# Kernel tuning notes

Measured on AMD Instinct MI355X. Metric: run time of the kernel, lower is better.

Reference implementation:

```python
import jax, jax.numpy as jnp
import numpy as np

H = 4          # num_heads (= num_kv_heads, num_kv_groups = 1)
DK = 256       # head_k_dim
DV = 256       # head_v_dim
M = 256        # num_slots
GATE_NORM = 16.0
EPS = 1e-5


def _rmsnorm(x, w):
    var = jnp.mean(jnp.square(x), axis=-1, keepdims=True)
    return x * jax.lax.rsqrt(var + EPS) * w


def _swish(x):
    return x * jax.nn.sigmoid(x)


def setup_inputs() -> dict:
    key = jax.random.key(0)
    ks = jax.random.split(key, 8)
    B, T, D = 4, 2048, 1024
    scale = 2 ** (-2.5) * (2.0 / (D + D)) ** 0.5 * (3.0 ** 0.5) * 2  # ~xavier*gain magnitude
    return {
        "hidden_states": jax.random.normal(ks[0], (B, T, D), jnp.float32),
        "norm_weight": jnp.ones((D,), jnp.float32),
        "w_q": jax.random.normal(ks[1], (D, D), jnp.float32) * scale,
        "w_k": jax.random.normal(ks[2], (D, D), jnp.float32) * scale,
        "w_v": jax.random.normal(ks[3], (D, D), jnp.float32) * scale,
        "w_f": jax.random.normal(ks[4], (H * M, D), jnp.float32) * scale,
        "gnorm_weight": jnp.ones((D,), jnp.float32),
        "w_o": jax.random.normal(ks[5], (D, D), jnp.float32) * scale,
    }


def _gsa_scan(q, k, v, s, g):
    # all inputs time-major: q [T,B,H,DK], k [T,B,H,DK], v [T,B,H,DV],
    # s [T,B,H,M] (slot write strength), g [T,B,H,M] (log forget gate)
    B, Hh = q.shape[1], q.shape[2]
    Hk0 = jnp.zeros((B, Hh, DK, M), q.dtype)
    Hv0 = jnp.zeros((B, Hh, M, DV), q.dtype)

    def step(carry, xs):
        Hk, Hv = carry
        qt, kt, vt, st, gt = xs
        lam = jnp.exp(gt)                                       # [B,H,M]
        # pass 1: linear attn over slots (gate on value/slot dim)
        Hk = Hk * lam[:, :, None, :] + kt[..., :, None] * st[..., None, :]
        z = jnp.einsum('bhk,bhkm->bhm', qt, Hk)                 # slot logits
        p = jax.nn.softmax(z, axis=-1)                          # slot read weights
        # pass 2: linear attn from slots to values (gate on key/slot dim)
        Hv = Hv * lam[..., :, None] + st[..., :, None] * vt[..., None, :]
        ot = jnp.einsum('bhm,bhmv->bhv', p, Hv)
        return (Hk, Hv), ot

    _, o = jax.lax.scan(step, (Hk0, Hv0), (q, k, v, s, g))
    return o  # [T,B,H,DV]


def reference(hidden_states, norm_weight, w_q, w_k, w_v, w_f, gnorm_weight, w_o):
    B, T, D = hidden_states.shape
    h = _rmsnorm(hidden_states, norm_weight)                    # norm_first
    q = _swish(h @ w_q.T).reshape(B, T, H, DK)                  # swish feature map
    k = _swish(h @ w_k.T).reshape(B, T, H, DK)
    v = _swish(h @ w_v.T).reshape(B, T, H, DV)
    f = jax.nn.log_sigmoid(h @ w_f.T).reshape(B, T, H, M) / GATE_NORM
    s = 1.0 - jnp.exp(f)
    tm = lambda x: jnp.transpose(x, (1, 0, 2, 3))               # [B,T,H,*] -> [T,B,H,*]
    o = _gsa_scan(tm(q), tm(k), tm(v), tm(s), tm(f))            # [T,B,H,DV]
    o = jnp.transpose(o, (1, 0, 2, 3)).reshape(B, T, H * DV)
    # use_norm & no output gate: swish -> RMSNorm -> o_proj
    o = _swish(o)
    o = _rmsnorm(o, gnorm_weight)
    return o @ w_o.T
```

## Files before the change

### kernel.cpp

```cpp
#include <hip/hip_runtime.h>
#include <hip/hip_bf16.h>

typedef unsigned short u16;
typedef unsigned int u32;

using bf16x8 = __bf16 __attribute__((ext_vector_type(8)));
using s16x8  = short  __attribute__((ext_vector_type(8)));
using f32x4  = float  __attribute__((ext_vector_type(4)));

#define DEV static __device__ __forceinline__

constexpr int T_ = 2048, D_ = 1024;
constexpr int C_ = 64, NC_ = 32;
constexpr float EPS_ = 1e-5f;

DEV float bf2f(u16 u) { return __uint_as_float(((u32)u) << 16); }
DEV u16 f2bf(float f) {
  u32 u = __float_as_uint(f);
  return (u16)((u + 0x7fffu + ((u >> 16) & 1u)) >> 16);
}
DEV float swishf(float x) { return x / (1.f + __expf(-x)); }
DEV f32x4 zero4() { f32x4 z = {0.f, 0.f, 0.f, 0.f}; return z; }

DEV bf16x8 ld8(const u16* p, int ld, int r0, int k0, int lane) {
  return *(const bf16x8*)(p + (size_t)(r0 + (lane & 15)) * ld +
                          (size_t)(k0 + ((lane >> 4) << 3)));
}
DEV f32x4 MFMA(bf16x8 a, bf16x8 b, f32x4 c) {
  return __builtin_amdgcn_mfma_f32_16x16x32_bf16(a, b, c, 0, 0, 0);
}
DEV void gld_lds16(const void* g, void* l) {
  __builtin_amdgcn_global_load_lds(
      (const __attribute__((address_space(1))) unsigned int*)g,
      (__attribute__((address_space(3))) unsigned int*)l, 16, 0, 0);
}

__global__ __launch_bounds__(256) void k_cvt5(
    const float* __restrict__ s0, const float* __restrict__ s1,
    const float* __restrict__ s2, const float* __restrict__ s3,
    const float* __restrict__ s4, u16* __restrict__ d0, u16* __restrict__ d1,
    u16* __restrict__ d2, u16* __restrict__ d3, u16* __restrict__ d4) {
  const int wsel = blockIdx.x >> 10;
  const float* s = (wsel == 0) ? s0 : (wsel == 1) ? s1 : (wsel == 2) ? s2
                   : (wsel == 3) ? s3 : s4;
  u16* d = (wsel == 0) ? d0 : (wsel == 1) ? d1 : (wsel == 2) ? d2
           : (wsel == 3) ? d3 : d4;
  const int i = (blockIdx.x & 1023) * 256 + threadIdx.x;
  float4 v = ((const float4*)s)[i];
  uint2 o;
  o.x = (u32)f2bf(v.x) | ((u32)f2bf(v.y) << 16);
  o.y = (u32)f2bf(v.z) | ((u32)f2bf(v.w) << 16);
  ((uint2*)d)[i] = o;
}

__global__ __launch_bounds__(256) void k_rmsnorm(const float* __restrict__ x,
                                                 const float* __restrict__ w,
                                                 u16* __restrict__ h) {
  const int row = blockIdx.x, tid = threadIdx.x;
  float4 v = ((const float4*)(x + (size_t)row * D_))[tid];
  float ss = v.x * v.x + v.y * v.y + v.z * v.z + v.w * v.w;
#pragma unroll
  for (int d = 32; d >= 1; d >>= 1) ss += __shfl_xor(ss, d, 64);
  __shared__ float red[4];
  if ((tid & 63) == 0) red[tid >> 6] = ss;
  __syncthreads();
  float rs = rsqrtf((red[0] + red[1] + red[2] + red[3]) * (1.f / D_) + EPS_);
  float4 wv = ((const float4*)w)[tid];
  uint2 o;
  o.x = (u32)f2bf(v.x * rs * wv.x) | ((u32)f2bf(v.y * rs * wv.y) << 16);
  o.y = (u32)f2bf(v.z * rs * wv.z) | ((u32)f2bf(v.w * rs * wv.w) << 16);
  *(uint2*)(h + (size_t)row * D_ + tid * 4) = o;
}

__global__ __launch_bounds__(256) void k_swishnorm(const u16* __restrict__ x,
                                                   const float* __restrict__ w,
                                                   u16* __restrict__ o) {
  const int row = blockIdx.x, tid = threadIdx.x;
  uint2 pk = *(const uint2*)(x + (size_t)row * D_ + tid * 4);
  float v0 = swishf(bf2f((u16)(pk.x & 0xffff))), v1 = swishf(bf2f((u16)(pk.x >> 16)));
  float v2 = swishf(bf2f((u16)(pk.y & 0xffff))), v3 = swishf(bf2f((u16)(pk.y >> 16)));
  float ss = v0 * v0 + v1 * v1 + v2 * v2 + v3 * v3;
#pragma unroll
  for (int d = 32; d >= 1; d >>= 1) ss += __shfl_xor(ss, d, 64);
  __shared__ float red[4];
  if ((tid & 63) == 0) red[tid >> 6] = ss;
  __syncthreads();
  float rs = rsqrtf((red[0] + red[1] + red[2] + red[3]) * (1.f / D_) + EPS_);
  float4 wv = ((const float4*)w)[tid];
  uint2 ov;
  ov.x = (u32)f2bf(v0 * rs * wv.x) | ((u32)f2bf(v1 * rs * wv.y) << 16);
  ov.y = (u32)f2bf(v2 * rs * wv.z) | ((u32)f2bf(v3 * rs * wv.w) << 16);
  *(uint2*)(o + (size_t)row * D_ + tid * 4) = ov;
}

#define WAITV6() asm volatile("s_waitcnt vmcnt(6)" ::: "memory")
#define WAITV0() asm volatile("s_waitcnt vmcnt(0)" ::: "memory")
__global__ __launch_bounds__(256, 2) void k_gemm4(
    const u16* __restrict__ A, const u16* __restrict__ w0,
    const u16* __restrict__ w1, const u16* __restrict__ w2,
    const u16* __restrict__ w3, u16* __restrict__ oq, u16* __restrict__ okk,
    u16* __restrict__ ov, float* __restrict__ og, const int mb) {
  __shared__ __align__(16) u16 As[3][128 * 32];
  __shared__ __align__(16) u16 Bs[3][4][64 * 32];
  const int m0 = mb + blockIdx.x * 128, n0 = blockIdx.y * 64;
  const int tid = threadIdx.x, lane = tid & 63, wvi = tid >> 6;
  f32x4 acc[4][2][4];
#pragma unroll
  for (int w = 0; w < 4; w++)
#pragma unroll
    for (int i = 0; i < 2; i++)
#pragma unroll
      for (int j = 0; j < 4; j++) acc[w][i][j] = zero4();
  const int srow = tid >> 2, scb = (tid & 3) * 8;
  const u16* Ag = A + (size_t)(m0 + srow) * 1024 + scb;
  const u16* Wg0 = w0 + (size_t)(n0 + srow) * 1024 + scb;
  const u16* Wg1 = w1 + (size_t)(n0 + srow) * 1024 + scb;
  const u16* Wg2 = w2 + (size_t)(n0 + srow) * 1024 + scb;
  const u16* Wg3 = w3 + (size_t)(n0 + srow) * 1024 + scb;
  const int sofs = (wvi * 16) * 32;

  auto stage = [&](int buf, int kk) {
    gld_lds16(Ag + kk, &As[buf][sofs]);
    gld_lds16(Ag + kk + 64 * 1024, &As[buf][sofs + 64 * 32]);
    gld_lds16(Wg0 + kk, &Bs[buf][0][sofs]);
    gld_lds16(Wg1 + kk, &Bs[buf][1][sofs]);
    gld_lds16(Wg2 + kk, &Bs[buf][2][sofs]);
    gld_lds16(Wg3 + kk, &Bs[buf][3][sofs]);
  };
  auto compute = [&](int buf) {
    bf16x8 af[2];
#pragma unroll
    for (int i = 0; i < 2; i++)
      af[i] = ld8(As[buf], 32, wvi * 32 + 16 * i, 0, lane);
#pragma unroll
    for (int w = 0; w < 4; w++) {
      bf16x8 bfr[4];
#pragma unroll
      for (int j = 0; j < 4; j++) bfr[j] = ld8(Bs[buf][w], 32, 16 * j, 0, lane);
#pragma unroll
      for (int i = 0; i < 2; i++)
#pragma unroll
        for (int j = 0; j < 4; j++) acc[w][i][j] = MFMA(af[i], bfr[j], acc[w][i][j]);
    }
  };

  stage(0, 0);
  stage(1, 32);
  int b0 = 0, b1 = 1, b2 = 2;
  for (int t = 0; t < 32; ++t) {
    if (t < 31) { WAITV6(); } else { WAITV0(); }
    __builtin_amdgcn_sched_barrier(0);
    __builtin_amdgcn_s_barrier();
    __builtin_amdgcn_sched_barrier(0);
    if (t + 2 < 32) stage(b2, (t + 2) * 32);
    __builtin_amdgcn_s_setprio(1);
    compute(b0);
    __builtin_amdgcn_s_setprio(0);
    int tmp = b0; b0 = b1; b1 = b2; b2 = tmp;
  }
  const int q4 = lane >> 4, c15 = lane & 15;
#pragma unroll
  for (int w = 0; w < 4; w++)
#pragma unroll
    for (int i = 0; i < 2; i++)
#pragma unroll
      for (int j = 0; j < 4; j++)
#pragma unroll
        for (int r = 0; r < 4; r++) {
          int grow = m0 + wvi * 32 + 16 * i + 4 * q4 + r;
          int gcol = n0 + 16 * j + c15;
          size_t idx = (size_t)grow * 1024 + gcol;
          float val = acc[w][i][j][r];
          if (w < 3) {
            u16* o = (w == 0) ? oq : (w == 1) ? okk : ov;
            o[idx] = f2bf(swishf(val));
          } else {
            float g = (val >= 0.f) ? -log1pf(__expf(-val))
                                   : (val - log1pf(__expf(val)));
            og[idx] = g * (1.0f / 16.0f);
          }
        }
}

__global__ __launch_bounds__(256) void k_gemmO(const u16* __restrict__ A,
                                               const u16* __restrict__ W,
                                               float* __restrict__ ofin) {
  __shared__ __align__(16) u16 As[128 * 32];
  __shared__ __align__(16) u16 Bs[128 * 32];
  const int m0 = blockIdx.x * 128, n0 = blockIdx.y * 128;
  const int tid = threadIdx.x, lane = tid & 63, wvi = tid >> 6;
  const int wr = wvi >> 1, wc = wvi & 1;
  f32x4 acc[4][4];
#pragma unroll
  for (int i = 0; i < 4; i++)
#pragma unroll
    for (int j = 0; j < 4; j++) acc[i][j] = zero4();
  const int srow = tid >> 2, scb = (tid & 3) * 8;
  const u16* Ag = A + (size_t)(m0 + srow) * 1024 + scb;
  const u16* Wg = W + (size_t)(n0 + srow) * 1024 + scb;
  u16* AsW = As + (wvi * 16) * 32;
  u16* BsW = Bs + (wvi * 16) * 32;
  for (int kk = 0; kk < 1024; kk += 32) {
    gld_lds16(Ag + kk, AsW);
    gld_lds16(Ag + kk + 64 * 1024, AsW + 64 * 32);
    gld_lds16(Wg + kk, BsW);
    gld_lds16(Wg + kk + 64 * 1024, BsW + 64 * 32);
    __syncthreads();
    bf16x8 af[4], bfr[4];
#pragma unroll
    for (int i = 0; i < 4; i++) af[i] = ld8(As, 32, wr * 64 + 16 * i, 0, lane);
#pragma unroll
    for (int j = 0; j < 4; j++) bfr[j] = ld8(Bs, 32, wc * 64 + 16 * j, 0, lane);
#pragma unroll
    for (int i = 0; i < 4; i++)
#pragma unroll
      for (int j = 0; j < 4; j++) acc[i][j] = MFMA(af[i], bfr[j], acc[i][j]);
    __syncthreads();
  }
  const int q4 = lane >> 4, c15 = lane & 15;
#pragma unroll
  for (int i = 0; i < 4; i++)
#pragma unroll
    for (int j = 0; j < 4; j++)
#pragma unroll
      for (int r = 0; r < 4; r++) {
        int grow = m0 + wr * 64 + 16 * i + 4 * q4 + r;
        int gcol = n0 + wc * 64 + 16 * j + c15;
        ofin[(size_t)grow * 1024 + gcol] = acc[i][j][r];
      }
}

__global__ __launch_bounds__(256) void k_gates(float* __restrict__ g_inout,
                                               u16* __restrict__ U_t,
                                               float* __restrict__ Lam) {
  const int c = blockIdx.x, p = blockIdx.y, tid = threadIdx.x;
  const int b = p >> 2, hh = p & 3;
  const int R0 = b * T_ + c * C_, hb = hh * 256;
  float ga = 0.f, ea = 1.f;
  short ubuf[C_];
#pragma unroll
  for (int t = 0; t < C_; t++) {
    size_t gi = (size_t)(R0 + t) * D_ + hb + tid;
    float gv = g_inout[gi];
    ga += gv;
    ea = __expf(ga);
    ubuf[t] = (short)f2bf((1.f - __expf(gv)) * __expf(-ga));
    g_inout[gi] = ea;
  }
  Lam[((size_t)p * NC_ + c) * 256 + tid] = ea;
  u16* up = U_t + ((size_t)p * NC_ + c) * (256 * C_) + (size_t)tid * C_;
#pragma unroll
  for (int i = 0; i < 8; i++) {
    s16x8 w;
#pragma unroll
    for (int j = 0; j < 8; j++) w[j] = ubuf[i * 8 + j];
    *(s16x8*)(up + i * 8) = w;
  }
}

__global__ __launch_bounds__(256) void k_intra(
    const u16* __restrict__ kg, const u16* __restrict__ vg,
    const u16* __restrict__ U_t, const float* __restrict__ Lam,
    u16* __restrict__ Sk, u16* __restrict__ Sv) {
  __shared__ __align__(16) u16 KV[256 * 72];
  __shared__ float LamH[256];
  const int c = blockIdx.x, p = blockIdx.y;
  const int b = p >> 2, hh = p & 3;
  const int R0 = b * T_ + c * C_, hb = hh * 256;
  const int tid = threadIdx.x, lane = tid & 63, wvi = tid >> 6;
  const int q4 = lane >> 4, c15 = lane & 15;
  const size_t chunk = (size_t)p * NC_ + c;
  const u16* Uc = U_t + chunk * (256 * C_);
  const size_t scBase = chunk * (256 * 256);

  LamH[tid] = Lam[chunk * 256 + tid];
  for (int t = 0; t < C_; t++)
    KV[tid * 72 + t] = kg[(size_t)(R0 + t) * D_ + hb + tid];
  __syncthreads();

  for (int cb = 0; cb < 4; cb++) {
    f32x4 acc[4][4];
#pragma unroll
    for (int i = 0; i < 4; i++)
#pragma unroll
      for (int j = 0; j < 4; j++) acc[i][j] = zero4();
#pragma unroll
    for (int ks = 0; ks < 2; ks++) {
      bf16x8 af[4], bfr[4];
#pragma unroll
      for (int i = 0; i < 4; i++) af[i] = ld8(Uc, C_, 64 * wvi + 16 * i, 32 * ks, lane);
#pragma unroll
      for (int j = 0; j < 4; j++) bfr[j] = ld8(KV, 72, 64 * cb + 16 * j, 32 * ks, lane);
#pragma unroll
      for (int i = 0; i < 4; i++)
#pragma unroll
        for (int j = 0; j < 4; j++) acc[i][j] = MFMA(af[i], bfr[j], acc[i][j]);
    }
#pragma unroll
    for (int i = 0; i < 4; i++)
#pragma unroll
      for (int j = 0; j < 4; j++)
#pragma unroll
        for (int r = 0; r < 4; r++) {
          int ml = 64 * wvi + 16 * i + 4 * q4 + r;
          int dd = 64 * cb + 16 * j + c15;
          Sk[scBase + (size_t)ml * 256 + dd] = f2bf(acc[i][j][r] * LamH[ml]);
        }
  }
  __syncthreads();

  for (int t = 0; t < C_; t++)
    KV[tid * 72 + t] = vg[(size_t)(R0 + t) * D_ + hb + tid];
  __syncthreads();

  for (int cb = 0; cb < 4; cb++) {
    f32x4 acc[4][4];
#pragma unroll
    for (int i = 0; i < 4; i++)
#pragma unroll
      for (int j = 0; j < 4; j++) acc[i][j] = zero4();
#pragma unroll
    for (int ks = 0; ks < 2; ks++) {
      bf16x8 af[4], bfr[4];
#pragma unroll
      for (int i = 0; i < 4; i++) af[i] = ld8(KV, 72, 64 * wvi + 16 * i, 32 * ks, lane);
#pragma unroll
      for (int j = 0; j < 4; j++) bfr[j] = ld8(Uc, C_, 64 * cb + 16 * j, 32 * ks, lane);
#pragma unroll
      for (int i = 0; i < 4; i++)
#pragma unroll
        for (int j = 0; j < 4; j++) acc[i][j] = MFMA(af[i], bfr[j], acc[i][j]);
    }
#pragma unroll
    for (int i = 0; i < 4; i++)
#pragma unroll
      for (int j = 0; j < 4; j++)
#pragma unroll
        for (int r = 0; r < 4; r++) {
          int vv = 64 * wvi + 16 * i + 4 * q4 + r;
          int ml = 64 * cb + 16 * j + c15;
          Sv[scBase + (size_t)vv * 256 + ml] = f2bf(acc[i][j][r] * LamH[ml]);
        }
  }
}

__global__ __launch_bounds__(256) void k_scan(u16* __restrict__ Sk,
                                              u16* __restrict__ Sv,
                                              const float* __restrict__ Lam) {
  const int gid = blockIdx.x * 256 + threadIdx.x;
  const int st = gid >> 17;
  const int w = gid & 131071;
  const int p = w >> 13;
  const int r = (w >> 5) & 255;
  const int c0 = (w & 31) * 8;
  u16* S = st ? Sv : Sk;
  const size_t base = (size_t)p * NC_ * 65536 + (size_t)r * 256 + c0;
  const float* Lp = Lam + (size_t)p * NC_ * 256;
  float acc[8] = {0, 0, 0, 0, 0, 0, 0, 0};
  for (int c = 0; c < NC_; c++) {
    s16x8 in = *(const s16x8*)(S + base + (size_t)c * 65536);
    s16x8 ov;
#pragma unroll
    for (int j = 0; j < 8; j++) ov[j] = (short)f2bf(acc[j]);
    *(s16x8*)(S + base + (size_t)c * 65536) = ov;
    if (st == 0) {
      float lam = Lp[c * 256 + r];
#pragma unroll
      for (int j = 0; j < 8; j++) acc[j] = acc[j] * lam + bf2f((u16)in[j]);
    } else {
#pragma unroll
      for (int j = 0; j < 8; j++) {
        float lam = Lp[c * 256 + c0 + j];
        acc[j] = acc[j] * lam + bf2f((u16)in[j]);
      }
    }
  }
}

__global__ __launch_bounds__(256) void k_out(
    const u16* __restrict__ qg, const u16* __restrict__ kg,
    const u16* __restrict__ vg, const u16* __restrict__ U_t,
    const float* __restrict__ Eg, const u16* __restrict__ Sk,
    const u16* __restrict__ Sv, u16* __restrict__ orw) {
  __shared__ __align__(16) char lds[52224];
  u16* As = (u16*)lds;
  u16* Pt = (u16*)(lds + 9216);
  u16* UnH = (u16*)(lds + 43008);
  u16* VxH = (u16*)(lds + 43008);

  const int c = blockIdx.x, p = blockIdx.y;
  const int b = p >> 2, hh = p & 3;
  const int R0 = b * T_ + c * C_, hb = hh * 256;
  const int tid = threadIdx.x, lane = tid & 63, wvi = tid >> 6;
  const int q4 = lane >> 4, c15 = lane & 15;
  const u16* qbase = qg + (size_t)R0 * D_ + hb;
  const u16* kbase = kg + (size_t)R0 * D_ + hb;
  const float* Ebase = Eg + (size_t)R0 * D_ + hb;
  const size_t chunk = (size_t)p * NC_ + c;
  const u16* SkC = Sk + chunk * 65536;
  const u16* SvC = Sv + chunk * 65536;
  const u16* Uc = U_t + chunk * (256 * C_);

  {
    f32x4 acc[4];
#pragma unroll
    for (int n = 0; n < 4; n++) acc[n] = zero4();
#pragma unroll
    for (int ks = 0; ks < 8; ks++) {
      bf16x8 af = ld8(qbase, D_, 16 * wvi, 32 * ks, lane);
#pragma unroll
      for (int n = 0; n < 4; n++)
        acc[n] = MFMA(af, ld8(kbase, D_, 16 * n, 32 * ks, lane), acc[n]);
    }
#pragma unroll
    for (int n = 0; n < 4; n++)
#pragma unroll
      for (int r = 0; r < 4; r++) {
        int t = 16 * wvi + 4 * q4 + r, tau = 16 * n + c15;
        As[t * 72 + tau] = f2bf(tau <= t ? acc[n][r] : 0.f);
      }
  }
  __syncthreads();

  f32x4 zac[16];
#pragma unroll
  for (int mh = 0; mh < 2; mh++) {
#pragma unroll
    for (int n = 0; n < 8; n++) zac[mh * 8 + n] = zero4();
#pragma unroll
    for (int ks = 0; ks < 2; ks++) {
      bf16x8 af = ld8(As, 72, 16 * wvi, 32 * ks, lane);
#pragma unroll
      for (int n = 0; n < 8; n++)
        zac[mh * 8 + n] = MFMA(af, ld8(Uc, C_, mh * 128 + 16 * n, 32 * ks, lane),
                               zac[mh * 8 + n]);
    }
#pragma unroll
    for (int ks = 0; ks < 8; ks++) {
      bf16x8 af = ld8(qbase, D_, 16 * wvi, 32 * ks, lane);
#pragma unroll
      for (int n = 0; n < 8; n++)
        zac[mh * 8 + n] = MFMA(
            af, ld8(SkC + (size_t)mh * 128 * 256, 256, 16 * n, 32 * ks, lane),
            zac[mh * 8 + n]);
    }
#pragma unroll
    for (int n = 0; n < 8; n++)
#pragma unroll
      for (int r = 0; r < 4; r++) {
        int t = 16 * wvi + 4 * q4 + r;
        zac[mh * 8 + n][r] *= Ebase[(size_t)t * D_ + mh * 128 + 16 * n + c15];
      }
  }

  float invR[4];
#pragma unroll
  for (int r = 0; r < 4; r++) {
    float mx = -3.0e38f;
#pragma unroll
    for (int i = 0; i < 16; i++) mx = fmaxf(mx, zac[i][r]);
    mx = fmaxf(mx, __shfl_xor(mx, 1, 64));
    mx = fmaxf(mx, __shfl_xor(mx, 2, 64));
    mx = fmaxf(mx, __shfl_xor(mx, 4, 64));
    mx = fmaxf(mx, __shfl_xor(mx, 8, 64));
    float sm = 0.f;
#pragma unroll
    for (int i = 0; i < 16; i++) {
      float e = __expf(zac[i][r] - mx);
      zac[i][r] = e;
      sm += e;
    }
    sm += __shfl_xor(sm, 1, 64);
    sm += __shfl_xor(sm, 2, 64);
    sm += __shfl_xor(sm, 4, 64);
    sm += __shfl_xor(sm, 8, 64);
    invR[r] = 1.f / sm;
  }
#pragma unroll
  for (int i = 0; i < 16; i++)
#pragma unroll
    for (int r = 0; r < 4; r++) {
      int t = 16 * wvi + 4 * q4 + r;
      int m = (i >> 3) * 128 + 16 * (i & 7) + c15;
      float e = Ebase[(size_t)t * D_ + m];
      Pt[t * 264 + m] = f2bf(zac[i][r] * invR[r] * e);
    }
  __syncthreads();

  {
    f32x4 wac[4];
#pragma unroll
    for (int n = 0; n < 4; n++) wac[n] = zero4();
    for (int mq = 0; mq < 4; mq++) {
      {
        int mloc = tid >> 2, th = tid & 3;
        const u16* ur = Uc + (size_t)(mq * 64 + mloc) * C_ + th * 16;
#pragma unroll
        for (int tt = 0; tt < 2; tt++) {
          s16x8 v = *(const s16x8*)(ur + tt * 8);
#pragma unroll
          for (int j = 0; j < 8; j++)
            UnH[(th * 16 + tt * 8 + j) * 72 + mloc] = (u16)v[j];
        }
      }
      __syncthreads();
#pragma unroll
      for (int ks = 0; ks < 2; ks++) {
        bf16x8 af = ld8(Pt, 264, 16 * wvi, mq * 64 + 32 * ks, lane);
#pragma unroll
        for (int n = 0; n < 4; n++)
          wac[n] = MFMA(af, ld8(UnH, 72, 16 * n, 32 * ks, lane), wac[n]);
      }
      __syncthreads();
    }
#pragma unroll
    for (int n = 0; n < 4; n++)
#pragma unroll
      for (int r = 0; r < 4; r++) {
        int t = 16 * wvi + 4 * q4 + r, tau = 16 * n + c15;
        As[t * 72 + tau] = f2bf(tau <= t ? wac[n][r] : 0.f);
      }
  }
  __syncthreads();

  for (int vq = 0; vq < 4; vq++) {
    {
      int vloc = tid >> 2, th = tid & 3;
#pragma unroll 4
      for (int tt = 0; tt < 16; tt++) {
        int t = th * 16 + tt;
        VxH[vloc * 72 + t] = vg[(size_t)(R0 + t) * D_ + hb + vq * 64 + vloc];
      }
    }
    __syncthreads();
    f32x4 oac[4];
#pragma unroll
    for (int n = 0; n < 4; n++) oac[n] = zero4();
#pragma unroll
    for (int ks = 0; ks < 8; ks++) {
      bf16x8 af = ld8(Pt, 264, 16 * wvi, 32 * ks, lane);
#pragma unroll
      for (int n = 0; n < 4; n++)
        oac[n] = MFMA(af, ld8(SvC + (size_t)vq * 64 * 256, 256, 16 * n, 32 * ks, lane), oac[n]);
    }
#pragma unroll
    for (int ks = 0; ks < 2; ks++) {
      bf16x8 af = ld8(As, 72, 16 * wvi, 32 * ks, lane);
#pragma unroll
      for (int n = 0; n < 4; n++)
        oac[n] = MFMA(af, ld8(VxH, 72, 16 * n, 32 * ks, lane), oac[n]);
    }
#pragma unroll
    for (int n = 0; n < 4; n++)
#pragma unroll
      for (int r = 0; r < 4; r++) {
        int t = 16 * wvi + 4 * q4 + r;
        int vc = vq * 64 + 16 * n + c15;
        orw[(size_t)(R0 + t) * D_ + hb + vc] = f2bf(oac[n][r]);
      }
    __syncthreads();
  }
}

extern "C" void kernel_launch(void* const* d_in, const int* in_sizes, int n_in,
                              void* d_out, int out_size, void* d_ws, size_t ws_size,
                              hipStream_t stream) {
  (void)in_sizes; (void)n_in; (void)out_size; (void)ws_size;
  const float* x   = (const float*)d_in[0];
  const float* nw  = (const float*)d_in[1];
  const float* wq  = (const float*)d_in[2];
  const float* wk  = (const float*)d_in[3];
  const float* wvp = (const float*)d_in[4];
  const float* wf  = (const float*)d_in[5];
  const float* gw  = (const float*)d_in[6];
  const float* wo  = (const float*)d_in[7];
  float* out = (float*)d_out;
  char* ws = (char*)d_ws;
  const size_t MB = 1024ull * 1024ull;
  u16*   hbuf = (u16*)(ws);
  u16*   qb   = (u16*)(ws + 16 * MB);
  u16*   kb   = (u16*)(ws + 32 * MB);
  u16*   vb   = (u16*)(ws + 48 * MB);
  float* gb   = (float*)(ws + 64 * MB);
  u16*   SkB  = (u16*)(ws + 96 * MB);
  u16*   SvB  = (u16*)(ws + 160 * MB);
  float* Lam  = (float*)(ws + 224 * MB);
  u16*   orw  = (u16*)(ws + 226 * MB);
  u16*   wqb  = (u16*)(ws + 242 * MB);
  u16*   wkb  = (u16*)(ws + 244 * MB);
  u16*   wvb  = (u16*)(ws + 246 * MB);
  u16*   wfb  = (u16*)(ws + 248 * MB);
  u16*   wob  = (u16*)(ws + 250 * MB);
  u16*   U_t  = hbuf;

  k_cvt5<<<dim3(5120), dim3(256), 0, stream>>>(wq, wk, wvp, wf, wo,
                                               wqb, wkb, wvb, wfb, wob);
  k_rmsnorm<<<dim3(8192), dim3(256), 0, stream>>>(x, nw, hbuf);
  k_gemm4<<<dim3(32, 16), dim3(256), 0, stream>>>(
      hbuf, wqb, wkb, wvb, wfb, qb, kb, vb, gb, 0);
  k_gemm4<<<dim3(32, 16), dim3(256), 0, stream>>>(
      hbuf, wqb, wkb, wvb, wfb, qb, kb, vb, gb, 4096);
  k_gates<<<dim3(NC_, 16), dim3(256), 0, stream>>>(gb, U_t, Lam);
  k_intra<<<dim3(NC_, 16), dim3(256), 0, stream>>>(kb, vb, U_t, Lam, SkB, SvB);
  k_scan<<<dim3(1024), dim3(256), 0, stream>>>(SkB, SvB, Lam);
  k_out<<<dim3(NC_, 16), dim3(256), 0, stream>>>(qb, kb, vb, U_t, gb, SkB, SvB, orw);
  k_swishnorm<<<dim3(8192), dim3(256), 0, stream>>>(orw, gw, hbuf);
  k_gemmO<<<dim3(64, 8), dim3(256), 0, stream>>>(hbuf, wob, out);
}
```

Measured before the change: 481.9 us.

## Split k_out work across eight waves with cross-wave softmax merge

Doubles the k_out block to 512 threads so two wave groups each handle half of the slot and value columns. The softmax over 256 slots is split, and the two halves' max and sum are combined through shared memory. This cuts the per-wave accumulator count, which should lower register pressure and raise latency hiding in a grid of only 512 blocks. In exchange it adds an extra barrier and a larger LDS footprint.

```diff
diff --git a/kernel.cpp b/kernel.cpp
--- a/kernel.cpp
+++ b/kernel.cpp
@@ -377,21 +377,24 @@
   }
 }
 
-__global__ __launch_bounds__(256) void k_out(
+__global__ __launch_bounds__(512) void k_out(
     const u16* __restrict__ qg, const u16* __restrict__ kg,
     const u16* __restrict__ vg, const u16* __restrict__ U_t,
     const float* __restrict__ Eg, const u16* __restrict__ Sk,
     const u16* __restrict__ Sv, u16* __restrict__ orw) {
-  __shared__ __align__(16) char lds[52224];
-  u16* As = (u16*)lds;
-  u16* Pt = (u16*)(lds + 9216);
-  u16* UnH = (u16*)(lds + 43008);
-  u16* VxH = (u16*)(lds + 43008);
+  __shared__ __align__(16) char lds[62464];
+  u16* As  = (u16*)lds;
+  u16* Pt  = (u16*)(lds + 9216);
+  float* SM = (float*)(lds + 43008);
+  u16* Ust = (u16*)(lds + 44032);
+  u16* Vst0 = (u16*)(lds + 44032);
+  u16* Vst1 = (u16*)(lds + 53248);
 
   const int c = blockIdx.x, p = blockIdx.y;
   const int b = p >> 2, hh = p & 3;
   const int R0 = b * T_ + c * C_, hb = hh * 256;
   const int tid = threadIdx.x, lane = tid & 63, wvi = tid >> 6;
+  const int tw = wvi & 3, gh = wvi >> 2;
   const int q4 = lane >> 4, c15 = lane & 15;
   const u16* qbase = qg + (size_t)R0 * D_ + hb;
   const u16* kbase = kg + (size_t)R0 * D_ + hb;
@@ -402,70 +405,64 @@
   const u16* Uc = U_t + chunk * (256 * C_);
 
   {
-    f32x4 acc[4];
-#pragma unroll
-    for (int n = 0; n < 4; n++) acc[n] = zero4();
+    f32x4 acc[2];
+    acc[0] = zero4(); acc[1] = zero4();
 #pragma unroll
     for (int ks = 0; ks < 8; ks++) {
-      bf16x8 af = ld8(qbase, D_, 16 * wvi, 32 * ks, lane);
-#pragma unroll
-      for (int n = 0; n < 4; n++)
-        acc[n] = MFMA(af, ld8(kbase, D_, 16 * n, 32 * ks, lane), acc[n]);
-    }
-#pragma unroll
-    for (int n = 0; n < 4; n++)
+      bf16x8 af = ld8(qbase, D_, 16 * tw, 32 * ks, lane);
+#pragma unroll
+      for (int n = 0; n < 2; n++)
+        acc[n] = MFMA(af, ld8(kbase, D_, 16 * (2 * gh + n), 32 * ks, lane), acc[n]);
+    }
+#pragma unroll
+    for (int n = 0; n < 2; n++)
 #pragma unroll
       for (int r = 0; r < 4; r++) {
-        int t = 16 * wvi + 4 * q4 + r, tau = 16 * n + c15;
+        int t = 16 * tw + 4 * q4 + r, tau = 16 * (2 * gh + n) + c15;
         As[t * 72 + tau] = f2bf(tau <= t ? acc[n][r] : 0.f);
       }
   }
   __syncthreads();
 
-  f32x4 zac[16];
-#pragma unroll
-  for (int mh = 0; mh < 2; mh++) {
-#pragma unroll
-    for (int n = 0; n < 8; n++) zac[mh * 8 + n] = zero4();
-#pragma unroll
-    for (int ks = 0; ks < 2; ks++) {
-      bf16x8 af = ld8(As, 72, 16 * wvi, 32 * ks, lane);
-#pragma unroll
-      for (int n = 0; n < 8; n++)
-        zac[mh * 8 + n] = MFMA(af, ld8(Uc, C_, mh * 128 + 16 * n, 32 * ks, lane),
-                               zac[mh * 8 + n]);
-    }
-#pragma unroll
-    for (int ks = 0; ks < 8; ks++) {
-      bf16x8 af = ld8(qbase, D_, 16 * wvi, 32 * ks, lane);
-#pragma unroll
-      for (int n = 0; n < 8; n++)
-        zac[mh * 8 + n] = MFMA(
-            af, ld8(SkC + (size_t)mh * 128 * 256, 256, 16 * n, 32 * ks, lane),
-            zac[mh * 8 + n]);
-    }
+  f32x4 zac[8];
+#pragma unroll
+  for (int n = 0; n < 8; n++) zac[n] = zero4();
+#pragma unroll
+  for (int ks = 0; ks < 2; ks++) {
+    bf16x8 af = ld8(As, 72, 16 * tw, 32 * ks, lane);
 #pragma unroll
     for (int n = 0; n < 8; n++)
-#pragma unroll
-      for (int r = 0; r < 4; r++) {
-        int t = 16 * wvi + 4 * q4 + r;
-        zac[mh * 8 + n][r] *= Ebase[(size_t)t * D_ + mh * 128 + 16 * n + c15];
-      }
-  }
-
-  float invR[4];
+      zac[n] = MFMA(af, ld8(Uc, C_, gh * 128 + 16 * n, 32 * ks, lane), zac[n]);
+  }
+#pragma unroll
+  for (int ks = 0; ks < 8; ks++) {
+    bf16x8 af = ld8(qbase, D_, 16 * tw, 32 * ks, lane);
+#pragma unroll
+    for (int n = 0; n < 8; n++)
+      zac[n] = MFMA(af, ld8(SkC + (size_t)gh * 128 * 256, 256, 16 * n, 32 * ks, lane),
+                    zac[n]);
+  }
+#pragma unroll
+  for (int n = 0; n < 8; n++)
+#pragma unroll
+    for (int r = 0; r < 4; r++) {
+      int t = 16 * tw + 4 * q4 + r;
+      zac[n][r] *= Ebase[(size_t)t * D_ + gh * 128 + 16 * n + c15];
+    }
+
+  float pmx[4], psm[4];
 #pragma unroll
   for (int r = 0; r < 4; r++) {
     float mx = -3.0e38f;
 #pragma unroll
-    for (int i = 0; i < 16; i++) mx = fmaxf(mx, zac[i][r]);
+    for (int i = 0; i < 8; i++) mx = fmaxf(mx, zac[i][r]);
     mx = fmaxf(mx, __shfl_xor(mx, 1, 64));
     mx = fmaxf(mx, __shfl_xor(mx, 2, 64));
     mx = fmaxf(mx, __shfl_xor(mx, 4, 64));
     mx = fmaxf(mx, __shfl_xor(mx, 8, 64));
     float sm = 0.f;
 #pragma unroll
-    for (int i = 0; i < 16; i++) {
+    for (int i = 0; i < 8; i++) {
       float e = __expf(zac[i][r] - mx);
       zac[i][r] = e;
       sm += e;
@@ -474,91 +471,104 @@
     sm += __shfl_xor(sm, 2, 64);
     sm += __shfl_xor(sm, 4, 64);
     sm += __shfl_xor(sm, 8, 64);
-    invR[r] = 1.f / sm;
-  }
-#pragma unroll
-  for (int i = 0; i < 16; i++)
-#pragma unroll
-    for (int r = 0; r < 4; r++) {
-      int t = 16 * wvi + 4 * q4 + r;
-      int m = (i >> 3) * 128 + 16 * (i & 7) + c15;
+    pmx[r] = mx; psm[r] = sm;
+    if (c15 == 0) {
+      int t = 16 * tw + 4 * q4 + r;
+      SM[t * 4 + gh * 2]     = mx;
+      SM[t * 4 + gh * 2 + 1] = sm;
+    }
+  }
+  __syncthreads();
+#pragma unroll
+  for (int r = 0; r < 4; r++) {
+    int t = 16 * tw + 4 * q4 + r;
+    float mxo = SM[t * 4 + (1 - gh) * 2];
+    float smo = SM[t * 4 + (1 - gh) * 2 + 1];
+    float gmx = fmaxf(pmx[r], mxo);
+    float sc = __expf(pmx[r] - gmx) /
+               (psm[r] * __expf(pmx[r] - gmx) + smo * __expf(mxo - gmx));
+#pragma unroll
+    for (int n = 0; n < 8; n++) {
+      int m = gh * 128 + 16 * n + c15;
       float e = Ebase[(size_t)t * D_ + m];
-      Pt[t * 264 + m] = f2bf(zac[i][r] * invR[r] * e);
-    }
+      Pt[t * 264 + m] = f2bf(zac[n][r] * sc * e);
+    }
+  }
   __syncthreads();
 
   {
-    f32x4 wac[4];
-#pragma unroll
-    for (int n = 0; n < 4; n++) wac[n] = zero4();
+    f32x4 wac[2];
+    wac[0] = zero4(); wac[1] = zero4();
     for (int mq = 0; mq < 4; mq++) {
       {
-        int mloc = tid >> 2, th = tid & 3;
-        const u16* ur = Uc + (size_t)(mq * 64 + mloc) * C_ + th * 16;
-#pragma unroll
-        for (int tt = 0; tt < 2; tt++) {
-          s16x8 v = *(const s16x8*)(ur + tt * 8);
-#pragma unroll
-          for (int j = 0; j < 8; j++)
-            UnH[(th * 16 + tt * 8 + j) * 72 + mloc] = (u16)v[j];
+        int mloc = tid >> 3, th = tid & 7;
+        s16x8 v = *(const s16x8*)(Uc + (size_t)(mq * 64 + mloc) * C_ + th * 8);
+#pragma unroll
+        for (int j = 0; j < 8; j++)
+          Ust[(th * 8 + j) * 72 + mloc] = (u16)v[j];
+      }
+      __syncthreads();
+#pragma unroll
+      for (int ks = 0; ks < 2; ks++) {
+        bf16x8 af = ld8(Pt, 264, 16 * tw, mq * 64 + 32 * ks, lane);
+#pragma unroll
+        for (int n = 0; n < 2; n++)
+          wac[n] = MFMA(af, ld8(Ust, 72, 16 * (2 * gh + n), 32 * ks, lane), wac[n]);
+      }
+      __syncthreads();
+    }
+#pragma unroll
+    for (int n = 0; n < 2; n++)
+#pragma unroll
+      for (int r = 0; r < 4; r++) {
+        int t = 16 * tw + 4 * q4 + r, tau = 16 * (2 * gh + n) + c15;
+        As[t * 72 + tau] = f2bf(tau <= t ? wac[n][r] : 0.f);
+      }
+  }
+  __syncthreads();
+
+  {
+    u16* Vst = gh ? Vst1 : Vst0;
+    const int lt = tid & 255;
+    for (int q = 0; q < 2; q++) {
+      const int vq = 2 * gh + q;
+      {
+        int vloc = lt >> 2, th = lt & 3;
+#pragma unroll 4
+        for (int tt = 0; tt < 16; tt++) {
+          int t = th * 16 + tt;
+          Vst[vloc * 72 + t] = vg[(size_t)(R0 + t) * D_ + hb + vq * 64 + vloc];
         }
       }
       __syncthreads();
+      f32x4 oac[4];
+#pragma unroll
+      for (int n = 0; n < 4; n++) oac[n] = zero4();
+#pragma unroll
+      for (int ks = 0; ks < 8; ks++) {
+        bf16x8 af = ld8(Pt, 264, 16 * tw, 32 * ks, lane);
+#pragma unroll
+        for (int n = 0; n < 4; n++)
+          oac[n] = MFMA(af, ld8(SvC + (size_t)vq * 64 * 256, 256, 16 * n, 32 * ks, lane),
+                        oac[n]);
+      }
 #pragma unroll
       for (int ks = 0; ks < 2; ks++) {
-        bf16x8 af = ld8(Pt, 264, 16 * wvi, mq * 64 + 32 * ks, lane);
+        bf16x8 af = ld8(As, 72, 16 * tw, 32 * ks, lane);
 #pragma unroll
         for (int n = 0; n < 4; n++)
-          wac[n] = MFMA(af, ld8(UnH, 72, 16 * n, 32 * ks, lane), wac[n]);
-      }
+          oac[n] = MFMA(af, ld8(Vst, 72, 16 * n, 32 * ks, lane), oac[n]);
+      }
+#pragma unroll
+      for (int n = 0; n < 4; n++)
+#pragma unroll
+        for (int r = 0; r < 4; r++) {
+          int t = 16 * tw + 4 * q4 + r;
+          int vc = vq * 64 + 16 * n + c15;
+          orw[(size_t)(R0 + t) * D_ + hb + vc] = f2bf(oac[n][r]);
+        }
       __syncthreads();
     }
-#pragma unroll
-    for (int n = 0; n < 4; n++)
-#pragma unroll
-      for (int r = 0; r < 4; r++) {
-        int t = 16 * wvi + 4 * q4 + r, tau = 16 * n + c15;
-        As[t * 72 + tau] = f2bf(tau <= t ? wac[n][r] : 0.f);
-      }
-  }
-  __syncthreads();
-
-  for (int vq = 0; vq < 4; vq++) {
-    {
-      int vloc = tid >> 2, th = tid & 3;
-#pragma unroll 4
-      for (int tt = 0; tt < 16; tt++) {
-        int t = th * 16 + tt;
-        VxH[vloc * 72 + t] = vg[(size_t)(R0 + t) * D_ + hb + vq * 64 + vloc];
-      }
-    }
-    __syncthreads();
-    f32x4 oac[4];
-#pragma unroll
-    for (int n = 0; n < 4; n++) oac[n] = zero4();
-#pragma unroll
-    for (int ks = 0; ks < 8; ks++) {
-      bf16x8 af = ld8(Pt, 264, 16 * wvi, 32 * ks, lane);
-#pragma unroll
-      for (int n = 0; n < 4; n++)
-        oac[n] = MFMA(af, ld8(SvC + (size_t)vq * 64 * 256, 256, 16 * n, 32 * ks, lane), oac[n]);
-    }
-#pragma unroll
-    for (int ks = 0; ks < 2; ks++) {
-      bf16x8 af = ld8(As, 72, 16 * wvi, 32 * ks, lane);
-#pragma unroll
-      for (int n = 0; n < 4; n++)
-        oac[n] = MFMA(af, ld8(VxH, 72, 16 * n, 32 * ks, lane), oac[n]);
-    }
-#pragma unroll
-    for (int n = 0; n < 4; n++)
-#pragma unroll
-      for (int r = 0; r < 4; r++) {
-        int t = 16 * wvi + 4 * q4 + r;
-        int vc = vq * 64 + 16 * n + c15;
-        orw[(size_t)(R0 + t) * D_ + hb + vc] = f2bf(oac[n][r]);
-      }
-    __syncthreads();
   }
 }
 
@@ -603,7 +613,7 @@
   k_gates<<<dim3(NC_, 16), dim3(256), 0, stream>>>(gb, U_t, Lam);
   k_intra<<<dim3(NC_, 16), dim3(256), 0, stream>>>(kb, vb, U_t, Lam, SkB, SvB);
   k_scan<<<dim3(1024), dim3(256), 0, stream>>>(SkB, SvB, Lam);
-  k_out<<<dim3(NC_, 16), dim3(256), 0, stream>>>(qb, kb, vb, U_t, gb, SkB, SvB, orw);
+  k_out<<<dim3(NC_, 16), dim3(512), 0, stream>>>(qb, kb, vb, U_t, gb, SkB, SvB, orw);
   k_swishnorm<<<dim3(8192), dim3(256), 0, stream>>>(orw, gw, hbuf);
   k_gemmO<<<dim3(64, 8), dim3(256), 0, stream>>>(hbuf, wob, out);
 }
```

After: 486.8 us. Within noise of the previous version (+1.0%).
